# Performance work log

Measured on AMD Instinct MI355X. Metric: run time of the kernel, lower is better.

## Reference

```python
import jax, jax.numpy as jnp
import numpy as np
from jax import lax
from jax.scipy.special import logsumexp

B, T, H, L = 64, 512, 768, 9


def setup_inputs() -> dict:
    key = jax.random.key(0)
    k1, k2, k3, k4, k5 = jax.random.split(key, 5)
    hidden = jax.random.normal(k1, (B, T, H), dtype=jnp.float32)
    W = jax.random.normal(k2, (L, H), dtype=jnp.float32) * 0.02
    b = jnp.zeros((L,), dtype=jnp.float32)
    transitions = jax.random.normal(k3, (L, L), dtype=jnp.float32) * 0.1
    lengths = jax.random.randint(k4, (B,), T // 2, T + 1)
    seq_mask = jnp.arange(T)[None, :] < lengths[:, None]          # [B,T] bool
    labels = jax.random.randint(k5, (B, T), 0, L).astype(jnp.int32)
    labels = jnp.where(seq_mask, labels, -100).astype(jnp.int32)   # -100 = ignore
    attention_mask = seq_mask.astype(jnp.int32)
    return {"hidden": hidden, "W": W, "b": b, "transitions": transitions,
            "labels": labels, "attention_mask": attention_mask}


def _crf_nll(logits, tags, transitions, mask):
    # numerator: joint score of the gold path (no start/end transitions)
    maskf = mask.astype(logits.dtype)
    emit = jnp.take_along_axis(logits, tags[..., None], axis=2)[..., 0]   # [B,T]
    emit_score = (emit * maskf).sum(-1)
    trans = transitions[tags[:, :-1], tags[:, 1:]]                        # [B,T-1]
    trans_score = (trans * maskf[:, 1:]).sum(-1)
    numerator = emit_score + trans_score
    # denominator: forward algorithm (log-sum-exp recurrence over time)
    def step(alpha, xs):
        logit_t, mask_t = xs                                   # [B,L], [B]
        inner = alpha[:, :, None] + transitions[None, :, :] + logit_t[:, None, :]
        new = logsumexp(inner, axis=1)
        return jnp.where(mask_t[:, None], new, alpha), None
    alpha0 = logits[:, 0]                                      # mask[:,0] assumed True
    alpha, _ = lax.scan(step, alpha0,
                        (jnp.transpose(logits[:, 1:], (1, 0, 2)), mask[:, 1:].T))
    denominator = logsumexp(alpha, axis=-1)
    return -(numerator - denominator).sum()


def _viterbi(logits, transitions, mask):
    num_tags = transitions.shape[0]
    identity_bp = jnp.broadcast_to(jnp.arange(num_tags)[None, :], logits.shape[:1] + (num_tags,))

    def vstep(vscore, xs):
        logit_t, mask_t = xs
        inner = vscore[:, :, None] + transitions[None, :, :]   # [B,L_prev,L_cur]
        bp = jnp.argmax(inner, axis=1)                         # [B,L]
        new = jnp.max(inner, axis=1) + logit_t
        vscore = jnp.where(mask_t[:, None], new, vscore)
        bp = jnp.where(mask_t[:, None], bp, identity_bp)       # carry tag through pad
        return vscore, bp

    vscore0 = logits[:, 0]
    vscore, bps = lax.scan(vstep, vscore0,
                           (jnp.transpose(logits[:, 1:], (1, 0, 2)), mask[:, 1:].T))
    last_tag = jnp.argmax(vscore, axis=-1)                     # [B]

    def btstep(tag, bp_t):
        prev = jnp.take_along_axis(bp_t, tag[:, None], axis=1)[:, 0]
        return prev, tag

    first_tag, tags_rest = lax.scan(btstep, last_tag, bps, reverse=True)  # ys[t]=tag_{t+1}
    return jnp.concatenate([first_tag[:, None], tags_rest.T], axis=1)     # [B,T]


def reference(hidden, W, b, transitions, labels, attention_mask):
    mask = (attention_mask != 0) & (labels != -100)            # create_combined_mask
    logits = jnp.einsum('bth,lh->btl', hidden, W) + b          # classifier (dropout=eval)
    tags = jnp.where(labels == -100, 0, labels)                # adjust_labels_for_crf
    loss = _crf_nll(logits, tags, transitions, mask)           # -log_likelihood (summed)
    vtags = _viterbi(logits, transitions, mask)                # [B,T]
    # pad_predictions: prepend -100, shift right, -100 outside the masked span
    bsz = hidden.shape[0]
    neg = jnp.full((bsz, 1), -100, dtype=jnp.int32)
    shifted = jnp.concatenate([neg, vtags[:, :-1].astype(jnp.int32)], axis=1)
    valid = jnp.concatenate([jnp.zeros((bsz, 1), bool), mask[:, :-1]], axis=1)
    predictions = jnp.where(valid, shifted, -100)
    return loss, predictions
```

## Files before the change

kernel.cpp:

```cpp
#include <hip/hip_runtime.h>

#define BATCH 64
#define TLEN  512
#define HDIM  768
#define LTAGS 9

#define WS_LOGD 0
#define WS_LOGF 2359296
#define WS_VM   3538944
#define WS_AM   6193152
#define WS_NUM  6856704
#define WS_LOSS 6857216

__global__ __launch_bounds__(256) void logits_kernel(
    const float* __restrict__ hidden, const float* __restrict__ W,
    const float* __restrict__ bvec, double* __restrict__ logitsD,
    float* __restrict__ logitsF)
{
    __shared__ float sW[LTAGS * HDIM];
    __shared__ float sb[LTAGS];
    const int tid = threadIdx.x;
    for (int i = tid; i < LTAGS * HDIM; i += 256) sW[i] = W[i];
    if (tid < LTAGS) sb[tid] = bvec[tid];
    __syncthreads();

    const int lane = tid & 63;
    const int wave = tid >> 6;
    const int sub  = lane & 7;
    const int rg   = lane >> 3;

    const int rowBase = blockIdx.x * 64 + wave * 16;
    const int r0 = rowBase + rg;
    const int r1 = rowBase + rg + 8;
    const float* h0p = hidden + (size_t)r0 * HDIM;
    const float* h1p = hidden + (size_t)r1 * HDIM;

    double acc0[LTAGS], acc1[LTAGS];
    #pragma unroll
    for (int l = 0; l < LTAGS; ++l) { acc0[l] = 0.0; acc1[l] = 0.0; }

    #pragma unroll 2
    for (int i = 0; i < 24; ++i) {
        const int off = i * 32 + sub * 4;
        const float4 h0 = *(const float4*)(h0p + off);
        const float4 h1 = *(const float4*)(h1p + off);
        #pragma unroll
        for (int l = 0; l < LTAGS; ++l) {
            const float4 w = *(const float4*)&sW[l * HDIM + off];
            float d0 = h0.x * w.x;
            d0 = fmaf(h0.y, w.y, d0); d0 = fmaf(h0.z, w.z, d0); d0 = fmaf(h0.w, w.w, d0);
            float d1 = h1.x * w.x;
            d1 = fmaf(h1.y, w.y, d1); d1 = fmaf(h1.z, w.z, d1); d1 = fmaf(h1.w, w.w, d1);
            acc0[l] += (double)d0;
            acc1[l] += (double)d1;
        }
    }
    #pragma unroll
    for (int l = 0; l < LTAGS; ++l) {
        double v0 = acc0[l], v1 = acc1[l];
        #pragma unroll
        for (int off = 4; off > 0; off >>= 1) {
            v0 += __shfl_down(v0, off);
            v1 += __shfl_down(v1, off);
        }
        acc0[l] = v0; acc1[l] = v1;
    }
    if (sub == 0) {
        #pragma unroll
        for (int l = 0; l < LTAGS; ++l) {
            double v0 = acc0[l] + (double)sb[l];
            double v1 = acc1[l] + (double)sb[l];
            logitsD[(size_t)r0 * LTAGS + l] = v0;
            logitsD[(size_t)r1 * LTAGS + l] = v1;
            logitsF[(size_t)r0 * LTAGS + l] = (float)v0;
            logitsF[(size_t)r1 * LTAGS + l] = (float)v1;
        }
    }
}

__global__ __launch_bounds__(576) void crf1_kernel(
    const float* __restrict__ trans, const int* __restrict__ labels,
    const int* __restrict__ att, const double* __restrict__ logitsD,
    const float* __restrict__ logitsF,
    double* __restrict__ wsVM, float* __restrict__ wsAM,
    double* __restrict__ wsNum)
{
    __shared__ float  sLogF[513 * LTAGS];
    __shared__ double sT64[81];
    __shared__ float  sE32[81];
    __shared__ unsigned char sMk[513];
    __shared__ double sRedN[9];

    const int b = blockIdx.x, tid = threadIdx.x;

    const float* gF = logitsF + (size_t)b * TLEN * LTAGS;
    for (int i = tid; i < TLEN * LTAGS; i += 576) sLogF[i] = gF[i];
    if (tid < LTAGS) sLogF[TLEN * LTAGS + tid] = 0.f;
    if (tid < 81) { float tv = trans[tid]; sT64[tid] = (double)tv; sE32[tid] = __expf(tv); }

    const int* lab = labels + b * TLEN;
    const int* am  = att + b * TLEN;
    if (tid < TLEN) {
        int lv = lab[tid], av = am[tid];
        sMk[tid] = (av != 0 && lv != -100) ? 1 : 0;
    }
    if (tid == 0) sMk[TLEN] = 0;
    __syncthreads();

    double part = 0.0;
    if (tid < TLEN) {
        const int t = tid;
        int lv = lab[t];
        int tg = (lv == -100) ? 0 : lv;
        if (sMk[t]) part += logitsD[((size_t)b * TLEN + t) * LTAGS + tg];
        if (t < TLEN - 1 && sMk[t + 1]) {
            int lv2 = lab[t + 1];
            int tg2 = (lv2 == -100) ? 0 : lv2;
            part += (double)trans[tg * LTAGS + tg2];
        }
    }
    #pragma unroll
    for (int off = 32; off > 0; off >>= 1) part += __shfl_down(part, off);
    if ((tid & 63) == 0) sRedN[tid >> 6] = part;
    __syncthreads();
    if (tid == 0) {
        double s = 0.0;
        for (int w = 0; w < 8; ++w) s += sRedN[w];
        wsNum[b] = s;
    }

    {
        const int c = tid / 9, i = tid - 9 * c;
        double M[LTAGS];
        #pragma unroll
        for (int j = 0; j < LTAGS; ++j) M[j] = (i == j) ? 0.0 : -1e300;

        const double* lrow = logitsD + ((size_t)b * TLEN + (c * 8 + 1)) * LTAGS;
        double lg[LTAGS], lgN[LTAGS];
        #pragma unroll
        for (int j = 0; j < LTAGS; ++j) lg[j] = lrow[j];

        for (int s = 0; s < 8; ++s) {
            const int t = c * 8 + 1 + s;
            if (s < 7) {
                const double* ln = lrow + (s + 1) * LTAGS;
                #pragma unroll
                for (int j = 0; j < LTAGS; ++j) lgN[j] = ln[j];
            }
            const bool mk = (sMk[t] != 0);
            double nw[LTAGS];
            #pragma unroll
            for (int j = 0; j < LTAGS; ++j) {
                double bst = M[0] + sT64[j];
                #pragma unroll
                for (int k = 1; k < LTAGS; ++k) {
                    double cnd = M[k] + sT64[k * LTAGS + j];
                    bst = fmax(bst, cnd);
                }
                nw[j] = bst + lg[j];
            }
            #pragma unroll
            for (int j = 0; j < LTAGS; ++j) M[j] = mk ? nw[j] : M[j];
            #pragma unroll
            for (int j = 0; j < LTAGS; ++j) lg[j] = lgN[j];
        }
        double* dst = wsVM + (((size_t)b * 64 + c) * LTAGS + i) * LTAGS;
        #pragma unroll
        for (int j = 0; j < LTAGS; ++j) dst[j] = M[j];
    }

    if (tid < 288) {
        const int c = tid / 9, i = tid - 9 * c;
        float M[LTAGS];
        #pragma unroll
        for (int j = 0; j < LTAGS; ++j) M[j] = (i == j) ? 0.f : -1e30f;

        for (int s = 0; s < 16; ++s) {
            const int t = c * 16 + 1 + s;
            const bool mk = (sMk[t] != 0);
            float m = M[0];
            #pragma unroll
            for (int k = 1; k < LTAGS; ++k) m = fmaxf(m, M[k]);
            float P[LTAGS];
            #pragma unroll
            for (int k = 0; k < LTAGS; ++k) P[k] = __expf(M[k] - m);
            float nw[LTAGS];
            #pragma unroll
            for (int j = 0; j < LTAGS; ++j) {
                float sacc = P[0] * sE32[j];
                #pragma unroll
                for (int k = 1; k < LTAGS; ++k) sacc = fmaf(P[k], sE32[k * LTAGS + j], sacc);
                nw[j] = m + __logf(sacc) + sLogF[t * LTAGS + j];
            }
            #pragma unroll
            for (int j = 0; j < LTAGS; ++j) M[j] = mk ? nw[j] : M[j];
        }
        float* dst = wsAM + (((size_t)b * 32 + c) * LTAGS + i) * LTAGS;
        #pragma unroll
        for (int j = 0; j < LTAGS; ++j) dst[j] = M[j];
    }
}

__global__ __launch_bounds__(128) void crf2_kernel(
    const float* __restrict__ trans, const int* __restrict__ labels,
    const int* __restrict__ att, const double* __restrict__ logitsD,
    const double* __restrict__ wsVM, const float* __restrict__ wsAM,
    const double* __restrict__ wsNum, double* __restrict__ wsLoss,
    float* __restrict__ out)
{
    __shared__ double sVstart[65 * LTAGS];
    __shared__ unsigned long long sBPp[513];
    __shared__ unsigned long long sFmap[64];
    __shared__ int sTagB[65];
    __shared__ double sT64[81];
    __shared__ unsigned char sMk[513];
    __shared__ double sDen;
    __shared__ int sLast;

    const int b = blockIdx.x, tid = threadIdx.x;
    const int wave = tid >> 6, lane = tid & 63;
    const unsigned long long IDMAP = 0x876543210ull;

    const int* lab = labels + b * TLEN;
    const int* am  = att + b * TLEN;
    for (int t = tid; t < TLEN; t += 128) {
        int lv = lab[t], av = am[t];
        sMk[t] = (av != 0 && lv != -100) ? 1 : 0;
    }
    if (tid == 0) sMk[TLEN] = 0;
    if (tid < 81) sT64[tid] = (double)trans[tid];
    __syncthreads();

    if (wave == 0) {
        const int j = (lane < LTAGS) ? lane : (LTAGS - 1);
        double v = logitsD[(size_t)b * TLEN * LTAGS + j];
        const double* vmB = wsVM + (size_t)b * 64 * 81;
        double Mc[LTAGS], Mn[LTAGS];
        #pragma unroll
        for (int i = 0; i < LTAGS; ++i) Mc[i] = vmB[i * LTAGS + j];
        for (int c = 0; c < 64; ++c) {
            if (c < 63) {
                const double* p = vmB + (c + 1) * 81;
                #pragma unroll
                for (int i = 0; i < LTAGS; ++i) Mn[i] = p[i * LTAGS + j];
            }
            if (lane < LTAGS) sVstart[c * LTAGS + j] = v;
            double g[LTAGS];
            #pragma unroll
            for (int i = 0; i < LTAGS; ++i) g[i] = __shfl(v, i);
            double bst = g[0] + Mc[0];
            #pragma unroll
            for (int i = 1; i < LTAGS; ++i) bst = fmax(bst, g[i] + Mc[i]);
            v = bst;
            if (c < 63) {
                #pragma unroll
                for (int i = 0; i < LTAGS; ++i) Mc[i] = Mn[i];
            }
        }
        if (lane < LTAGS) sVstart[64 * LTAGS + j] = v;
        double g[LTAGS];
        #pragma unroll
        for (int i = 0; i < LTAGS; ++i) g[i] = __shfl(v, i);
        if (lane == 0) {
            int bi = 0; double bv = g[0];
            #pragma unroll
            for (int i = 1; i < LTAGS; ++i) if (g[i] > bv) { bv = g[i]; bi = i; }
            sLast = bi;
        }
    } else {
        const int j = (lane < LTAGS) ? lane : (LTAGS - 1);
        float v = (float)logitsD[(size_t)b * TLEN * LTAGS + j];
        const float* amB = wsAM + (size_t)b * 32 * 81;
        float Mc[LTAGS], Mn[LTAGS];
        #pragma unroll
        for (int i = 0; i < LTAGS; ++i) Mc[i] = amB[i * LTAGS + j];
        for (int c = 0; c < 32; ++c) {
            if (c < 31) {
                const float* p = amB + (c + 1) * 81;
                #pragma unroll
                for (int i = 0; i < LTAGS; ++i) Mn[i] = p[i * LTAGS + j];
            }
            float g[LTAGS];
            #pragma unroll
            for (int i = 0; i < LTAGS; ++i) g[i] = __shfl(v, i);
            float a[LTAGS];
            #pragma unroll
            for (int i = 0; i < LTAGS; ++i) a[i] = g[i] + Mc[i];
            float m = a[0];
            #pragma unroll
            for (int i = 1; i < LTAGS; ++i) m = fmaxf(m, a[i]);
            float sacc = 0.f;
            #pragma unroll
            for (int i = 0; i < LTAGS; ++i) sacc += __expf(a[i] - m);
            v = m + __logf(sacc);
            if (c < 31) {
                #pragma unroll
                for (int i = 0; i < LTAGS; ++i) Mc[i] = Mn[i];
            }
        }
        float g[LTAGS];
        #pragma unroll
        for (int i = 0; i < LTAGS; ++i) g[i] = __shfl(v, i);
        if (lane == 0) {
            float m = g[0];
            #pragma unroll
            for (int i = 1; i < LTAGS; ++i) m = fmaxf(m, g[i]);
            float sacc = 0.f;
            #pragma unroll
            for (int i = 0; i < LTAGS; ++i) sacc += __expf(g[i] - m);
            sDen = (double)(m + __logf(sacc));
        }
    }
    __syncthreads();

    if (tid < 64) {
        const int c = tid;
        double v[LTAGS];
        #pragma unroll
        for (int j = 0; j < LTAGS; ++j) v[j] = sVstart[c * LTAGS + j];
        const double* lrow = logitsD + ((size_t)b * TLEN + (c * 8 + 1)) * LTAGS;
        double lg[LTAGS], lgN[LTAGS];
        #pragma unroll
        for (int j = 0; j < LTAGS; ++j) lg[j] = lrow[j];

        for (int s = 0; s < 8; ++s) {
            const int t = c * 8 + 1 + s;
            if (s < 7) {
                const double* ln = lrow + (s + 1) * LTAGS;
                #pragma unroll
                for (int j = 0; j < LTAGS; ++j) lgN[j] = ln[j];
            }
            const bool mk = (sMk[t] != 0);
            unsigned long long pk = 0;
            double nv[LTAGS];
            #pragma unroll
            for (int j = 0; j < LTAGS; ++j) {
                double bst = v[0] + sT64[j];
                int bi = 0;
                #pragma unroll
                for (int k = 1; k < LTAGS; ++k) {
                    double cnd = v[k] + sT64[k * LTAGS + j];
                    bool gt = cnd > bst;
                    bst = gt ? cnd : bst;
                    bi  = gt ? k : bi;
                }
                nv[j] = bst + lg[j];
                pk |= ((unsigned long long)bi) << (4 * j);
            }
            pk = mk ? pk : IDMAP;
            sBPp[t] = pk;
            #pragma unroll
            for (int j = 0; j < LTAGS; ++j) v[j] = mk ? nv[j] : v[j];
            #pragma unroll
            for (int j = 0; j < LTAGS; ++j) lg[j] = lgN[j];
        }
        unsigned long long G = IDMAP;
        for (int s = 7; s >= 0; --s) {
            const unsigned long long bp = sBPp[c * 8 + 1 + s];
            unsigned long long ng = 0;
            #pragma unroll
            for (int j = 0; j < LTAGS; ++j) {
                int gj = (int)((G >> (4 * j)) & 15);
                int f  = (int)((bp >> (4 * gj)) & 15);
                ng |= ((unsigned long long)f) << (4 * j);
            }
            G = ng;
        }
        sFmap[c] = G;
    }
    __syncthreads();

    if (tid == 0) {
        int cur = sLast;
        sTagB[64] = cur;
        for (int c = 63; c >= 0; --c) {
            cur = (int)((sFmap[c] >> (4 * cur)) & 15);
            sTagB[c] = cur;
        }
    }
    __syncthreads();

    if (tid < 64) {
        const int c = tid;
        int cur = sTagB[c + 1];
        float* po = out + 1 + b * TLEN;
        for (int s = 8; s >= 1; --s) {
            const int t = c * 8 + s;
            if (t < TLEN) {
                int nxt = (int)((sBPp[t] >> (4 * cur)) & 15);
                po[t] = sMk[t - 1] ? (float)nxt : -100.f;
                cur = nxt;
            }
        }
    }
    if (tid == 0) {
        out[1 + b * TLEN] = -100.f;
        wsLoss[b] = sDen - wsNum[b];
    }
}

__global__ __launch_bounds__(64) void loss_kernel(
    const double* __restrict__ wsLoss, float* __restrict__ out)
{
    double v = wsLoss[threadIdx.x];
    #pragma unroll
    for (int off = 32; off > 0; off >>= 1) v += __shfl_down(v, off);
    if (threadIdx.x == 0) out[0] = (float)v;
}

extern "C" void kernel_launch(void* const* d_in, const int* in_sizes, int n_in,
                              void* d_out, int out_size, void* d_ws, size_t ws_size,
                              hipStream_t stream)
{
    const float* hidden = (const float*)d_in[0];
    const float* W      = (const float*)d_in[1];
    const float* bvec   = (const float*)d_in[2];
    const float* trans  = (const float*)d_in[3];
    const int*   labels = (const int*)d_in[4];
    const int*   att    = (const int*)d_in[5];
    float* out = (float*)d_out;

    char* ws = (char*)d_ws;
    double* logitsD = (double*)(ws + WS_LOGD);
    float*  logitsF = (float*)(ws + WS_LOGF);
    double* wsVM    = (double*)(ws + WS_VM);
    float*  wsAM    = (float*)(ws + WS_AM);
    double* wsNum   = (double*)(ws + WS_NUM);
    double* wsLoss  = (double*)(ws + WS_LOSS);

    logits_kernel<<<512, 256, 0, stream>>>(hidden, W, bvec, logitsD, logitsF);
    crf1_kernel<<<BATCH, 576, 0, stream>>>(trans, labels, att, logitsD, logitsF,
                                           wsVM, wsAM, wsNum);
    crf2_kernel<<<BATCH, 128, 0, stream>>>(trans, labels, att, logitsD,
                                           wsVM, wsAM, wsNum, wsLoss, out);
    loss_kernel<<<1, 64, 0, stream>>>(wsLoss, out);
}
```

Before: 262.8 us.

## Split CRF chunk work across 232 blocks, stage chunk maps in LDS, parallel-scan backtrace

The per-batch crf1 kernel is replaced by a flat chunk_kernel over 232 blocks. These blocks separately compute the Viterbi max-plus chunk matrices, the logsumexp chunk matrices and the gold-path numerator, so far more CUs are busy than with 64 blocks. Logits and masks are read straight from global memory, with the next step prefetched, instead of being staged in LDS. In crf2, the chunk matrices are first copied into shared memory with vector loads. The serial 64-step backtrace map composition becomes a wave-level shuffle prefix scan. This cuts latency on the sequential chain but adds a global-memory dependence in the chunk kernel.

```diff
diff --git a/kernel.cpp b/kernel.cpp
--- a/kernel.cpp
+++ b/kernel.cpp
@@ -78,76 +78,50 @@
     }
 }
 
-__global__ __launch_bounds__(576) void crf1_kernel(
+__global__ __launch_bounds__(256) void chunk_kernel(
     const float* __restrict__ trans, const int* __restrict__ labels,
     const int* __restrict__ att, const double* __restrict__ logitsD,
     const float* __restrict__ logitsF,
     double* __restrict__ wsVM, float* __restrict__ wsAM,
     double* __restrict__ wsNum)
 {
-    __shared__ float  sLogF[513 * LTAGS];
     __shared__ double sT64[81];
     __shared__ float  sE32[81];
-    __shared__ unsigned char sMk[513];
-    __shared__ double sRedN[9];
-
-    const int b = blockIdx.x, tid = threadIdx.x;
-
-    const float* gF = logitsF + (size_t)b * TLEN * LTAGS;
-    for (int i = tid; i < TLEN * LTAGS; i += 576) sLogF[i] = gF[i];
-    if (tid < LTAGS) sLogF[TLEN * LTAGS + tid] = 0.f;
+    const int tid = threadIdx.x;
     if (tid < 81) { float tv = trans[tid]; sT64[tid] = (double)tv; sE32[tid] = __expf(tv); }
-
-    const int* lab = labels + b * TLEN;
-    const int* am  = att + b * TLEN;
-    if (tid < TLEN) {
-        int lv = lab[tid], av = am[tid];
-        sMk[tid] = (av != 0 && lv != -100) ? 1 : 0;
-    }
-    if (tid == 0) sMk[TLEN] = 0;
     __syncthreads();
 
-    double part = 0.0;
-    if (tid < TLEN) {
-        const int t = tid;
-        int lv = lab[t];
-        int tg = (lv == -100) ? 0 : lv;
-        if (sMk[t]) part += logitsD[((size_t)b * TLEN + t) * LTAGS + tg];
-        if (t < TLEN - 1 && sMk[t + 1]) {
-            int lv2 = lab[t + 1];
-            int tg2 = (lv2 == -100) ? 0 : lv2;
-            part += (double)trans[tg * LTAGS + tg2];
-        }
-    }
-    #pragma unroll
-    for (int off = 32; off > 0; off >>= 1) part += __shfl_down(part, off);
-    if ((tid & 63) == 0) sRedN[tid >> 6] = part;
-    __syncthreads();
-    if (tid == 0) {
-        double s = 0.0;
-        for (int w = 0; w < 8; ++w) s += sRedN[w];
-        wsNum[b] = s;
-    }
-
-    {
-        const int c = tid / 9, i = tid - 9 * c;
+    const int blk = blockIdx.x;
+    if (blk < 144) {
+        const int gid = blk * 256 + tid;
+        const int b   = gid / 576;
+        const int rem = gid - b * 576;
+        const int c   = rem / 9;
+        const int i   = rem - c * 9;
+
         double M[LTAGS];
         #pragma unroll
         for (int j = 0; j < LTAGS; ++j) M[j] = (i == j) ? 0.0 : -1e300;
 
         const double* lrow = logitsD + ((size_t)b * TLEN + (c * 8 + 1)) * LTAGS;
+        const int* lab = labels + b * TLEN;
+        const int* am  = att + b * TLEN;
+        const int t0 = c * 8 + 1;
+
         double lg[LTAGS], lgN[LTAGS];
         #pragma unroll
         for (int j = 0; j < LTAGS; ++j) lg[j] = lrow[j];
+        bool mk = (am[t0] != 0) && (lab[t0] != -100);
 
         for (int s = 0; s < 8; ++s) {
-            const int t = c * 8 + 1 + s;
-            if (s < 7) {
+            bool mkN = false;
+            const int tn = t0 + s + 1;
+            if (s < 7 && tn <= TLEN - 1) {
                 const double* ln = lrow + (s + 1) * LTAGS;
                 #pragma unroll
                 for (int j = 0; j < LTAGS; ++j) lgN[j] = ln[j];
-            }
-            const bool mk = (sMk[t] != 0);
+                mkN = (am[tn] != 0) && (lab[tn] != -100);
+            }
             double nw[LTAGS];
             #pragma unroll
             for (int j = 0; j < LTAGS; ++j) {
@@ -160,24 +134,42 @@
                 nw[j] = bst + lg[j];
             }
             #pragma unroll
-            for (int j = 0; j < LTAGS; ++j) M[j] = mk ? nw[j] : M[j];
-            #pragma unroll
-            for (int j = 0; j < LTAGS; ++j) lg[j] = lgN[j];
+            for (int j = 0; j < LTAGS; ++j) { M[j] = mk ? nw[j] : M[j]; lg[j] = lgN[j]; }
+            mk = mkN;
         }
         double* dst = wsVM + (((size_t)b * 64 + c) * LTAGS + i) * LTAGS;
         #pragma unroll
         for (int j = 0; j < LTAGS; ++j) dst[j] = M[j];
-    }
-
-    if (tid < 288) {
-        const int c = tid / 9, i = tid - 9 * c;
+    } else if (blk < 216) {
+        const int gid = (blk - 144) * 256 + tid;
+        const int b   = gid / 288;
+        const int rem = gid - b * 288;
+        const int c   = rem / 9;
+        const int i   = rem - c * 9;
+
         float M[LTAGS];
         #pragma unroll
         for (int j = 0; j < LTAGS; ++j) M[j] = (i == j) ? 0.f : -1e30f;
 
+        const float* lrow = logitsF + ((size_t)b * TLEN + (c * 16 + 1)) * LTAGS;
+        const int* lab = labels + b * TLEN;
+        const int* am  = att + b * TLEN;
+        const int t0 = c * 16 + 1;
+
+        float lg[LTAGS], lgN[LTAGS];
+        #pragma unroll
+        for (int j = 0; j < LTAGS; ++j) lg[j] = lrow[j];
+        bool mk = (am[t0] != 0) && (lab[t0] != -100);
+
         for (int s = 0; s < 16; ++s) {
-            const int t = c * 16 + 1 + s;
-            const bool mk = (sMk[t] != 0);
+            bool mkN = false;
+            const int tn = t0 + s + 1;
+            if (s < 15 && tn <= TLEN - 1) {
+                const float* ln = lrow + (s + 1) * LTAGS;
+                #pragma unroll
+                for (int j = 0; j < LTAGS; ++j) lgN[j] = ln[j];
+                mkN = (am[tn] != 0) && (lab[tn] != -100);
+            }
             float m = M[0];
             #pragma unroll
             for (int k = 1; k < LTAGS; ++k) m = fmaxf(m, M[k]);
@@ -190,14 +182,39 @@
                 float sacc = P[0] * sE32[j];
                 #pragma unroll
                 for (int k = 1; k < LTAGS; ++k) sacc = fmaf(P[k], sE32[k * LTAGS + j], sacc);
-                nw[j] = m + __logf(sacc) + sLogF[t * LTAGS + j];
-            }
-            #pragma unroll
-            for (int j = 0; j < LTAGS; ++j) M[j] = mk ? nw[j] : M[j];
+                nw[j] = m + __logf(sacc) + lg[j];
+            }
+            #pragma unroll
+            for (int j = 0; j < LTAGS; ++j) { M[j] = mk ? nw[j] : M[j]; lg[j] = lgN[j]; }
+            mk = mkN;
         }
         float* dst = wsAM + (((size_t)b * 32 + c) * LTAGS + i) * LTAGS;
         #pragma unroll
         for (int j = 0; j < LTAGS; ++j) dst[j] = M[j];
+    } else {
+        const int bb   = (blk - 216) * 4 + (tid >> 6);
+        const int lane = tid & 63;
+        const int* lab = labels + bb * TLEN;
+        const int* am  = att + bb * TLEN;
+        const double* lrowb = logitsD + (size_t)bb * TLEN * LTAGS;
+        double part = 0.0;
+        #pragma unroll
+        for (int k = 0; k < 8; ++k) {
+            const int t = lane + k * 64;
+            int lv = lab[t], av = am[t];
+            bool mkc = (av != 0) && (lv != -100);
+            int tg = (lv == -100) ? 0 : lv;
+            if (mkc) part += lrowb[(size_t)t * LTAGS + tg];
+            if (t < TLEN - 1) {
+                int lv2 = lab[t + 1], av2 = am[t + 1];
+                bool mk2 = (av2 != 0) && (lv2 != -100);
+                int tg2 = (lv2 == -100) ? 0 : lv2;
+                if (mk2) part += sT64[tg * LTAGS + tg2];
+            }
+        }
+        #pragma unroll
+        for (int off = 32; off > 0; off >>= 1) part += __shfl_down(part, off);
+        if (lane == 0) wsNum[bb] = part;
     }
 }
 
@@ -208,9 +225,10 @@
     const double* __restrict__ wsNum, double* __restrict__ wsLoss,
     float* __restrict__ out)
 {
+    __shared__ __align__(16) double sVM[64 * 81];
+    __shared__ __align__(16) float  sAM[32 * 81];
     __shared__ double sVstart[65 * LTAGS];
     __shared__ unsigned long long sBPp[513];
-    __shared__ unsigned long long sFmap[64];
     __shared__ int sTagB[65];
     __shared__ double sT64[81];
     __shared__ unsigned char sMk[513];
@@ -221,6 +239,13 @@
     const int wave = tid >> 6, lane = tid & 63;
     const unsigned long long IDMAP = 0x876543210ull;
 
+    const double2* gVM = (const double2*)(wsVM + (size_t)b * 64 * 81);
+    double2* sVM2 = (double2*)sVM;
+    for (int i = tid; i < 2592; i += 128) sVM2[i] = gVM[i];
+    const float4* gAM = (const float4*)(wsAM + (size_t)b * 32 * 81);
+    float4* sAM4 = (float4*)sAM;
+    for (int i = tid; i < 648; i += 128) sAM4[i] = gAM[i];
+
     const int* lab = labels + b * TLEN;
     const int* am  = att + b * TLEN;
     for (int t = tid; t < TLEN; t += 128) {
@@ -234,15 +259,13 @@
     if (wave == 0) {
         const int j = (lane < LTAGS) ? lane : (LTAGS - 1);
         double v = logitsD[(size_t)b * TLEN * LTAGS + j];
-        const double* vmB = wsVM + (size_t)b * 64 * 81;
         double Mc[LTAGS], Mn[LTAGS];
         #pragma unroll
-        for (int i = 0; i < LTAGS; ++i) Mc[i] = vmB[i * LTAGS + j];
+        for (int i = 0; i < LTAGS; ++i) Mc[i] = sVM[i * LTAGS + j];
         for (int c = 0; c < 64; ++c) {
             if (c < 63) {
-                const double* p = vmB + (c + 1) * 81;
-                #pragma unroll
-                for (int i = 0; i < LTAGS; ++i) Mn[i] = p[i * LTAGS + j];
+                #pragma unroll
+                for (int i = 0; i < LTAGS; ++i) Mn[i] = sVM[(c + 1) * 81 + i * LTAGS + j];
             }
             if (lane < LTAGS) sVstart[c * LTAGS + j] = v;
             double g[LTAGS];
@@ -270,15 +293,13 @@
     } else {
         const int j = (lane < LTAGS) ? lane : (LTAGS - 1);
         float v = (float)logitsD[(size_t)b * TLEN * LTAGS + j];
-        const float* amB = wsAM + (size_t)b * 32 * 81;
         float Mc[LTAGS], Mn[LTAGS];
         #pragma unroll
-        for (int i = 0; i < LTAGS; ++i) Mc[i] = amB[i * LTAGS + j];
+        for (int i = 0; i < LTAGS; ++i) Mc[i] = sAM[i * LTAGS + j];
         for (int c = 0; c < 32; ++c) {
             if (c < 31) {
-                const float* p = amB + (c + 1) * 81;
-                #pragma unroll
-                for (int i = 0; i < LTAGS; ++i) Mn[i] = p[i * LTAGS + j];
+                #pragma unroll
+                for (int i = 0; i < LTAGS; ++i) Mn[i] = sAM[(c + 1) * 81 + i * LTAGS + j];
             }
             float g[LTAGS];
             #pragma unroll
@@ -313,6 +334,7 @@
     }
     __syncthreads();
 
+    unsigned long long S = IDMAP;
     if (tid < 64) {
         const int c = tid;
         double v[LTAGS];
@@ -325,7 +347,7 @@
 
         for (int s = 0; s < 8; ++s) {
             const int t = c * 8 + 1 + s;
-            if (s < 7) {
+            if (s < 7 && t + 1 <= TLEN - 1) {
                 const double* ln = lrow + (s + 1) * LTAGS;
                 #pragma unroll
                 for (int j = 0; j < LTAGS; ++j) lgN[j] = ln[j];
@@ -350,9 +372,7 @@
             pk = mk ? pk : IDMAP;
             sBPp[t] = pk;
             #pragma unroll
-            for (int j = 0; j < LTAGS; ++j) v[j] = mk ? nv[j] : v[j];
-            #pragma unroll
-            for (int j = 0; j < LTAGS; ++j) lg[j] = lgN[j];
+            for (int j = 0; j < LTAGS; ++j) { v[j] = mk ? nv[j] : v[j]; lg[j] = lgN[j]; }
         }
         unsigned long long G = IDMAP;
         for (int s = 7; s >= 0; --s) {
@@ -366,17 +386,27 @@
             }
             G = ng;
         }
-        sFmap[c] = G;
-    }
-    __syncthreads();
-
-    if (tid == 0) {
-        int cur = sLast;
-        sTagB[64] = cur;
-        for (int c = 63; c >= 0; --c) {
-            cur = (int)((sFmap[c] >> (4 * cur)) & 15);
-            sTagB[c] = cur;
-        }
+        S = G;
+    }
+
+    #pragma unroll
+    for (int d = 1; d < 64; d <<= 1) {
+        unsigned long long Sn = __shfl_down(S, d);
+        if (wave == 0 && lane + d < 64) {
+            unsigned long long R = 0;
+            #pragma unroll
+            for (int x = 0; x < LTAGS; ++x) {
+                int y = (int)((Sn >> (4 * x)) & 15);
+                int z = (int)((S >> (4 * y)) & 15);
+                R |= ((unsigned long long)z) << (4 * x);
+            }
+            S = R;
+        }
+    }
+    if (tid < 64) {
+        const int lt = sLast;
+        sTagB[tid] = (int)((S >> (4 * lt)) & 15);
+        if (tid == 0) sTagB[64] = lt;
     }
     __syncthreads();
 
@@ -429,8 +459,8 @@
     double* wsLoss  = (double*)(ws + WS_LOSS);
 
     logits_kernel<<<512, 256, 0, stream>>>(hidden, W, bvec, logitsD, logitsF);
-    crf1_kernel<<<BATCH, 576, 0, stream>>>(trans, labels, att, logitsD, logitsF,
-                                           wsVM, wsAM, wsNum);
+    chunk_kernel<<<232, 256, 0, stream>>>(trans, labels, att, logitsD, logitsF,
+                                          wsVM, wsAM, wsNum);
     crf2_kernel<<<BATCH, 128, 0, stream>>>(trans, labels, att, logitsD,
                                            wsVM, wsAM, wsNum, wsLoss, out);
     loss_kernel<<<1, 64, 0, stream>>>(wsLoss, out);
```

New measurement: 217.9 us. 17.1% less time.
